# Kernel optimization log

Hardware: AMD Instinct MI355X
Metric: run time of the kernel (lower is better)

Reference implementation:

```python
import jax, jax.numpy as jnp
import numpy as np

IN_DIM = 64
OUT_DIM = 64
NUM_SPLINES = 8
DEGREE = 3
EPS = 1e-8


def setup_inputs() -> dict:
    key = jax.random.key(0)
    k1, k2 = jax.random.split(key, 2)
    x = jax.random.normal(k1, (4, 512, IN_DIM), dtype=jnp.float32)
    control_points = jax.random.normal(k2, (OUT_DIM, IN_DIM, NUM_SPLINES), dtype=jnp.float32) * 0.1
    K = NUM_SPLINES + DEGREE + 1  # 12 knots
    knots = jnp.broadcast_to(jnp.linspace(-1.0, 1.0, K, dtype=jnp.float32), (OUT_DIM, IN_DIM, K)).copy()
    activation_weights = jnp.ones((OUT_DIM, IN_DIM, 4), dtype=jnp.float32) / 4.0
    return {"x": x, "control_points": control_points, "knots": knots, "activation_weights": activation_weights}


def _bspline_basis(x, knots, degree):
    # x: (b, n, d); knots: (O, d, K) -> basis (b, O, n, d, K-degree-1)
    xs = x[:, None, :, :, None]          # (b, 1, n, d, 1)
    t = knots[None, :, None, :, :]       # (1, O, 1, d, K)
    # Cox-de Boor degree 0: indicator of half-open knot interval
    B = ((xs >= t[..., :-1]) & (xs < t[..., 1:])).astype(x.dtype)  # (b, O, n, d, K-1)
    for k in range(1, degree + 1):
        Km = B.shape[-1]
        c1 = (xs - t[..., : Km - 1]) / (t[..., k : k + Km - 1] - t[..., : Km - 1] + EPS)
        c2 = (t[..., k + 1 : k + Km] - xs) / (t[..., k + 1 : k + Km] - t[..., 1:Km] + EPS)
        B = c1 * B[..., :-1] + c2 * B[..., 1:]
    return B


def reference(x, control_points, knots, activation_weights):
    # B-spline branch: (b,O,n,d,S) x (O,d,S) -> (b,O,n)
    basis = _bspline_basis(x, knots, DEGREE)
    out = jnp.einsum('bonds,ods->bon', basis, control_points)
    # activation-mixture branch: activations are independent of the out dim
    acts = jnp.stack([jax.nn.relu(x), jnp.tanh(x), jax.nn.sigmoid(x), x], axis=-1)  # (b,n,d,4)
    act_out = jnp.einsum('bnda,oda->bon', acts, activation_weights)
    return out + 0.1 * act_out  # (b, out_dim, n)
```

## Files before the change

kernel.cpp:

```cpp
#include <hip/hip_runtime.h>

#define D_IN 64
#define D_OUT 64
#define NS 8
#define NK 12
#define NF 12
#define KTOT (D_IN * NF)
#define KAN_EPS 1e-8f
#define NBN 2048
#define KSPLIT 8
#define KCH (KTOT / KSPLIT)

__device__ int g_mism[16];

#define F_ELEMS  (KTOT * NBN)
#define WT_ELEMS (KTOT * D_OUT)

__device__ inline void basis8(float xv, const float* __restrict__ t, float* __restrict__ B)
{
    float Bb[11];
    #pragma unroll
    for (int i = 0; i < 11; ++i) Bb[i] = (xv >= t[i] && xv < t[i + 1]) ? 1.f : 0.f;
    #pragma unroll
    for (int i = 0; i < 10; ++i)
        Bb[i] = (xv - t[i]) * (1.f / (t[i + 1] - t[i] + KAN_EPS)) * Bb[i]
              + (t[i + 2] - xv) * (1.f / (t[i + 2] - t[i + 1] + KAN_EPS)) * Bb[i + 1];
    #pragma unroll
    for (int i = 0; i < 9; ++i)
        Bb[i] = (xv - t[i]) * (1.f / (t[i + 2] - t[i] + KAN_EPS)) * Bb[i]
              + (t[i + 3] - xv) * (1.f / (t[i + 3] - t[i + 1] + KAN_EPS)) * Bb[i + 1];
    #pragma unroll
    for (int i = 0; i < 8; ++i)
        Bb[i] = (xv - t[i]) * (1.f / (t[i + 3] - t[i] + KAN_EPS)) * Bb[i]
              + (t[i + 4] - xv) * (1.f / (t[i + 4] - t[i + 1] + KAN_EPS)) * Bb[i + 1];
    #pragma unroll
    for (int i = 0; i < 8; ++i) B[i] = Bb[i];
}

__global__ __launch_bounds__(256)
void kan_prep(const float* __restrict__ cp,
              const float* __restrict__ knots,
              const float* __restrict__ aw,
              const float* __restrict__ x,
              float* __restrict__ F,
              float* __restrict__ Wt)
{
    const int blk = blockIdx.x;
    const int tid = threadIdx.x;

    if (blk < 512) {
        const int idx = blk * 256 + tid;
        const int d  = idx >> 11;
        const int bn = idx & 2047;
        const float xv = x[bn * D_IN + d];

        float t[NK];
        #pragma unroll
        for (int j = 0; j < NK; ++j) t[j] = knots[d * NK + j];

        float B[8];
        basis8(xv, t, B);

        float* __restrict__ Fr = F + d * NF * NBN + bn;
        #pragma unroll
        for (int s = 0; s < 8; ++s) Fr[s * NBN] = B[s];

        const float v  = __expf(-xv);
        const float Ra = __builtin_amdgcn_rcpf(1.f + v * v);
        const float Rb = __builtin_amdgcn_rcpf(1.f + v);
        Fr[8  * NBN] = fmaxf(xv, 0.f);
        Fr[9  * NBN] = 2.f * Ra - 1.f;
        Fr[10 * NBN] = Rb;
        Fr[11 * NBN] = xv;

    } else {
        const int od = (blk - 512) * 256 + tid;
        const int o = od >> 6, d = od & 63;
        #pragma unroll
        for (int s = 0; s < 8; ++s) Wt[(d * NF + s) * D_OUT + o] = cp[od * NS + s];
        #pragma unroll
        for (int a = 0; a < 4; ++a) Wt[(d * NF + 8 + a) * D_OUT + o] = 0.1f * aw[od * 4 + a];

        int m = 0;
        #pragma unroll
        for (int j = 0; j < NK; ++j)
            m |= (knots[od * NK + j] != knots[d * NK + j]) ? 1 : 0;
        __shared__ int sm;
        if (tid == 0) sm = 0;
        __syncthreads();
        if (m) atomicOr(&sm, 1);
        __syncthreads();
        if (tid == 0) g_mism[blk - 512] = sm;
    }
}

__global__ __launch_bounds__(512)
void kan_gemm(const float* __restrict__ F,
              const float* __restrict__ Wt,
              const float* __restrict__ knots,
              const float* __restrict__ cp,
              const float* __restrict__ aw,
              const float* __restrict__ x,
              float* __restrict__ partial)
{
    const int lane = threadIdx.x & 63;
    const int og   = __builtin_amdgcn_readfirstlane(threadIdx.x >> 6);
    const int bn   = blockIdx.x * 64 + lane;
    const int ks   = blockIdx.y;

    float acc[8] = {0.f, 0.f, 0.f, 0.f, 0.f, 0.f, 0.f, 0.f};

    int mm = 0;
    #pragma unroll
    for (int k = 0; k < 16; ++k) mm |= g_mism[k];

    if (mm == 0) {
        const float* __restrict__ Fp = F  + (size_t)(ks * KCH) * NBN + bn;
        const float* __restrict__ Wp = Wt + (ks * KCH) * D_OUT + og * 8;
        #pragma unroll 8
        for (int k = 0; k < KCH; ++k) {
            const float f = Fp[(size_t)k * NBN];
            #pragma unroll
            for (int j = 0; j < 8; ++j)
                acc[j] = fmaf(f, Wp[k * D_OUT + j], acc[j]);
        }
    } else {
        for (int d = ks * (KCH / NF); d < ks * (KCH / NF) + (KCH / NF); ++d) {
            const float xv = x[bn * D_IN + d];
            const float v  = __expf(-xv);
            const float Ra = __builtin_amdgcn_rcpf(1.f + v * v);
            const float Rb = __builtin_amdgcn_rcpf(1.f + v);
            const float fr = fmaxf(xv, 0.f), fth = 2.f * Ra - 1.f;
            #pragma unroll
            for (int j = 0; j < 8; ++j) {
                const int o  = og * 8 + j;
                const int od = o * D_IN + d;
                float t[NK];
                #pragma unroll
                for (int jj = 0; jj < NK; ++jj) t[jj] = knots[od * NK + jj];
                float B[8];
                basis8(xv, t, B);
                float sp = 0.f;
                #pragma unroll
                for (int s = 0; s < NS; ++s) sp += B[s] * cp[od * NS + s];
                sp += 0.1f * (aw[od * 4 + 0] * fr + aw[od * 4 + 1] * fth
                            + aw[od * 4 + 2] * Rb + aw[od * 4 + 3] * xv);
                acc[j] += sp;
            }
        }
    }

    float* __restrict__ pp = partial + ((size_t)ks * D_OUT + og * 8) * NBN + bn;
    #pragma unroll
    for (int j = 0; j < 8; ++j) pp[(size_t)j * NBN] = acc[j];
}

__global__ __launch_bounds__(256)
void kan_reduce(const float4* __restrict__ partial, float* __restrict__ out)
{
    const int q = blockIdx.x * 256 + threadIdx.x;
    float4 s = partial[q];
    #pragma unroll
    for (int ks = 1; ks < KSPLIT; ++ks) {
        const float4 p = partial[(size_t)ks * (D_OUT * NBN / 4) + q];
        s.x += p.x; s.y += p.y; s.z += p.z; s.w += p.w;
    }
    const int idx = q * 4;
    const int o  = idx >> 11;
    const int bn = idx & 2047;
    const int b  = bn >> 9;
    const int n  = bn & 511;
    *(float4*)&out[(((b << 6) + o) << 9) + n] = s;
}

extern "C" void kernel_launch(void* const* d_in, const int* in_sizes, int n_in,
                              void* d_out, int out_size, void* d_ws, size_t ws_size,
                              hipStream_t stream) {
    const float* x     = (const float*)d_in[0];
    const float* cp    = (const float*)d_in[1];
    const float* knots = (const float*)d_in[2];
    const float* aw    = (const float*)d_in[3];
    float* out = (float*)d_out;

    float* F       = (float*)d_ws;
    float* Wt      = F + F_ELEMS;
    float* partial = Wt + WT_ELEMS;

    kan_prep<<<528, 256, 0, stream>>>(cp, knots, aw, x, F, Wt);

    dim3 ggrid(NBN / 64, KSPLIT);
    kan_gemm<<<ggrid, 512, 0, stream>>>(F, Wt, knots, cp, aw, x, partial);

    kan_reduce<<<128, 256, 0, stream>>>((const float4*)partial, out);
}
```

Baseline: 24.55 us.

## Fuse prep, GEMM and reduce into one kernel with shared-memory tiles

The three launches (feature/weight prep, split-K GEMM, reduction) become one kernel. Each block builds its basis features and transposed weight slice directly in shared memory, runs the split-K GEMM from LDS, and the last block per bn-tile (found with an atomic counter) reduces the partials and writes the output. This removes two kernel launches and the global round-trip of the F and Wt buffers. In exchange, the knot-mismatch check becomes per-block over only its own d slice, and each block redundantly recomputes its weight slice.

Result: slower. 25.46 us (+3.7%).

```diff
diff --git a/kernel.cpp b/kernel.cpp
--- a/kernel.cpp
+++ b/kernel.cpp
@@ -5,16 +5,17 @@
 #define NS 8
 #define NK 12
 #define NF 12
-#define KTOT (D_IN * NF)
-#define KAN_EPS 1e-8f
 #define NBN 2048
 #define KSPLIT 8
-#define KCH (KTOT / KSPLIT)
+#define DCH 8
+#define KCH (DCH * NF)
+#define BNT 64
+#define NT (NBN / BNT)
+#define KAN_EPS 1e-8f
 
-__device__ int g_mism[16];
+__device__ int g_cnt[NT];
 
-#define F_ELEMS  (KTOT * NBN)
-#define WT_ELEMS (KTOT * D_OUT)
+__device__ inline float rcp_(float a) { return __builtin_amdgcn_rcpf(a); }
 
 __device__ inline void basis8(float xv, const float* __restrict__ t, float* __restrict__ B)
 {
@@ -23,123 +24,114 @@
     for (int i = 0; i < 11; ++i) Bb[i] = (xv >= t[i] && xv < t[i + 1]) ? 1.f : 0.f;
     #pragma unroll
     for (int i = 0; i < 10; ++i)
-        Bb[i] = (xv - t[i]) * (1.f / (t[i + 1] - t[i] + KAN_EPS)) * Bb[i]
-              + (t[i + 2] - xv) * (1.f / (t[i + 2] - t[i + 1] + KAN_EPS)) * Bb[i + 1];
+        Bb[i] = (xv - t[i]) * rcp_(t[i + 1] - t[i] + KAN_EPS) * Bb[i]
+              + (t[i + 2] - xv) * rcp_(t[i + 2] - t[i + 1] + KAN_EPS) * Bb[i + 1];
     #pragma unroll
     for (int i = 0; i < 9; ++i)
-        Bb[i] = (xv - t[i]) * (1.f / (t[i + 2] - t[i] + KAN_EPS)) * Bb[i]
-              + (t[i + 3] - xv) * (1.f / (t[i + 3] - t[i + 1] + KAN_EPS)) * Bb[i + 1];
+        Bb[i] = (xv - t[i]) * rcp_(t[i + 2] - t[i] + KAN_EPS) * Bb[i]
+              + (t[i + 3] - xv) * rcp_(t[i + 3] - t[i + 1] + KAN_EPS) * Bb[i + 1];
     #pragma unroll
     for (int i = 0; i < 8; ++i)
-        Bb[i] = (xv - t[i]) * (1.f / (t[i + 3] - t[i] + KAN_EPS)) * Bb[i]
-              + (t[i + 4] - xv) * (1.f / (t[i + 4] - t[i + 1] + KAN_EPS)) * Bb[i + 1];
+        Bb[i] = (xv - t[i]) * rcp_(t[i + 3] - t[i] + KAN_EPS) * Bb[i]
+              + (t[i + 4] - xv) * rcp_(t[i + 4] - t[i + 1] + KAN_EPS) * Bb[i + 1];
     #pragma unroll
     for (int i = 0; i < 8; ++i) B[i] = Bb[i];
 }
 
-__global__ __launch_bounds__(256)
-void kan_prep(const float* __restrict__ cp,
-              const float* __restrict__ knots,
-              const float* __restrict__ aw,
-              const float* __restrict__ x,
-              float* __restrict__ F,
-              float* __restrict__ Wt)
+__global__ __launch_bounds__(512)
+void kan_fused(const float* __restrict__ x,
+               const float* __restrict__ cp,
+               const float* __restrict__ knots,
+               const float* __restrict__ aw,
+               float* __restrict__ partial,
+               float* __restrict__ out)
 {
-    const int blk = blockIdx.x;
-    const int tid = threadIdx.x;
+    __shared__ float sF[KCH][BNT];
+    __shared__ float sW[KCH][D_OUT];
+    __shared__ int s_mism, s_last;
 
-    if (blk < 512) {
-        const int idx = blk * 256 + tid;
-        const int d  = idx >> 11;
-        const int bn = idx & 2047;
+    const int bt   = blockIdx.x;
+    const int ks   = blockIdx.y;
+    const int tid  = threadIdx.x;
+    const int lane = tid & 63;
+    const int wv   = __builtin_amdgcn_readfirstlane(tid >> 6);
+    const int d0   = ks * DCH;
+    const int bn   = bt * BNT + lane;
+
+    if (tid == 0) { s_mism = 0; }
+    __syncthreads();
+
+    {
+        const int d = d0 + wv;
         const float xv = x[bn * D_IN + d];
-
         float t[NK];
         #pragma unroll
         for (int j = 0; j < NK; ++j) t[j] = knots[d * NK + j];
-
         float B[8];
         basis8(xv, t, B);
+        #pragma unroll
+        for (int s = 0; s < 8; ++s) sF[wv * NF + s][lane] = B[s];
+        const float v = __expf(-xv);
+        sF[wv * NF + 8][lane]  = fmaxf(xv, 0.f);
+        sF[wv * NF + 9][lane]  = 2.f * rcp_(1.f + v * v) - 1.f;
+        sF[wv * NF + 10][lane] = rcp_(1.f + v);
+        sF[wv * NF + 11][lane] = xv;
+    }
 
-        float* __restrict__ Fr = F + d * NF * NBN + bn;
-        #pragma unroll
-        for (int s = 0; s < 8; ++s) Fr[s * NBN] = B[s];
-
-        const float v  = __expf(-xv);
-        const float Ra = __builtin_amdgcn_rcpf(1.f + v * v);
-        const float Rb = __builtin_amdgcn_rcpf(1.f + v);
-        Fr[8  * NBN] = fmaxf(xv, 0.f);
-        Fr[9  * NBN] = 2.f * Ra - 1.f;
-        Fr[10 * NBN] = Rb;
-        Fr[11 * NBN] = xv;
-
-    } else {
-        const int od = (blk - 512) * 256 + tid;
-        const int o = od >> 6, d = od & 63;
-        #pragma unroll
-        for (int s = 0; s < 8; ++s) Wt[(d * NF + s) * D_OUT + o] = cp[od * NS + s];
-        #pragma unroll
-        for (int a = 0; a < 4; ++a) Wt[(d * NF + 8 + a) * D_OUT + o] = 0.1f * aw[od * 4 + a];
+    {
+        const int dg = tid >> 6;
+        const int o  = lane;
+        const int d  = d0 + dg;
+        const int od = o * D_IN + d;
+        const float4 c0 = *(const float4*)&cp[od * NS];
+        const float4 c1 = *(const float4*)&cp[od * NS + 4];
+        const float4 av = *(const float4*)&aw[od * 4];
+        sW[dg * NF + 0][o] = c0.x;  sW[dg * NF + 1][o] = c0.y;
+        sW[dg * NF + 2][o] = c0.z;  sW[dg * NF + 3][o] = c0.w;
+        sW[dg * NF + 4][o] = c1.x;  sW[dg * NF + 5][o] = c1.y;
+        sW[dg * NF + 6][o] = c1.z;  sW[dg * NF + 7][o] = c1.w;
+        sW[dg * NF + 8][o]  = 0.1f * av.x;
+        sW[dg * NF + 9][o]  = 0.1f * av.y;
+        sW[dg * NF + 10][o] = 0.1f * av.z;
+        sW[dg * NF + 11][o] = 0.1f * av.w;
 
         int m = 0;
         #pragma unroll
         for (int j = 0; j < NK; ++j)
             m |= (knots[od * NK + j] != knots[d * NK + j]) ? 1 : 0;
-        __shared__ int sm;
-        if (tid == 0) sm = 0;
-        __syncthreads();
-        if (m) atomicOr(&sm, 1);
-        __syncthreads();
-        if (tid == 0) g_mism[blk - 512] = sm;
+        if (m) atomicOr(&s_mism, 1);
     }
-}
+    __syncthreads();
 
-__global__ __launch_bounds__(512)
-void kan_gemm(const float* __restrict__ F,
-              const float* __restrict__ Wt,
-              const float* __restrict__ knots,
-              const float* __restrict__ cp,
-              const float* __restrict__ aw,
-              const float* __restrict__ x,
-              float* __restrict__ partial)
-{
-    const int lane = threadIdx.x & 63;
-    const int og   = __builtin_amdgcn_readfirstlane(threadIdx.x >> 6);
-    const int bn   = blockIdx.x * 64 + lane;
-    const int ks   = blockIdx.y;
-
+    const int og8 = __builtin_amdgcn_readfirstlane(wv * 8);
     float acc[8] = {0.f, 0.f, 0.f, 0.f, 0.f, 0.f, 0.f, 0.f};
 
-    int mm = 0;
-    #pragma unroll
-    for (int k = 0; k < 16; ++k) mm |= g_mism[k];
-
-    if (mm == 0) {
-        const float* __restrict__ Fp = F  + (size_t)(ks * KCH) * NBN + bn;
-        const float* __restrict__ Wp = Wt + (ks * KCH) * D_OUT + og * 8;
-        #pragma unroll 8
+    if (s_mism == 0) {
+        #pragma unroll 4
         for (int k = 0; k < KCH; ++k) {
-            const float f = Fp[(size_t)k * NBN];
-            #pragma unroll
-            for (int j = 0; j < 8; ++j)
-                acc[j] = fmaf(f, Wp[k * D_OUT + j], acc[j]);
+            const float f   = sF[k][lane];
+            const float4 wA = *(const float4*)&sW[k][og8];
+            const float4 wB = *(const float4*)&sW[k][og8 + 4];
+            acc[0] = fmaf(f, wA.x, acc[0]);  acc[1] = fmaf(f, wA.y, acc[1]);
+            acc[2] = fmaf(f, wA.z, acc[2]);  acc[3] = fmaf(f, wA.w, acc[3]);
+            acc[4] = fmaf(f, wB.x, acc[4]);  acc[5] = fmaf(f, wB.y, acc[5]);
+            acc[6] = fmaf(f, wB.z, acc[6]);  acc[7] = fmaf(f, wB.w, acc[7]);
         }
     } else {
-        for (int d = ks * (KCH / NF); d < ks * (KCH / NF) + (KCH / NF); ++d) {
+        for (int dg = 0; dg < DCH; ++dg) {
+            const int d = d0 + dg;
             const float xv = x[bn * D_IN + d];
             const float v  = __expf(-xv);
-            const float Ra = __builtin_amdgcn_rcpf(1.f + v * v);
-            const float Rb = __builtin_amdgcn_rcpf(1.f + v);
+            const float Ra = rcp_(1.f + v * v), Rb = rcp_(1.f + v);
             const float fr = fmaxf(xv, 0.f), fth = 2.f * Ra - 1.f;
-            #pragma unroll
             for (int j = 0; j < 8; ++j) {
-                const int o  = og * 8 + j;
+                const int o  = og8 + j;
                 const int od = o * D_IN + d;
-                float t[NK];
+                float t2[NK];
                 #pragma unroll
-                for (int jj = 0; jj < NK; ++jj) t[jj] = knots[od * NK + jj];
+                for (int jj = 0; jj < NK; ++jj) t2[jj] = knots[od * NK + jj];
                 float B[8];
-                basis8(xv, t, B);
+                basis8(xv, t2, B);
                 float sp = 0.f;
                 #pragma unroll
                 for (int s = 0; s < NS; ++s) sp += B[s] * cp[od * NS + s];
@@ -150,27 +142,30 @@
         }
     }
 
-    float* __restrict__ pp = partial + ((size_t)ks * D_OUT + og * 8) * NBN + bn;
     #pragma unroll
-    for (int j = 0; j < 8; ++j) pp[(size_t)j * NBN] = acc[j];
-}
+    for (int j = 0; j < 8; ++j)
+        partial[(size_t)(ks * D_OUT + og8 + j) * NBN + bn] = acc[j];
 
-__global__ __launch_bounds__(256)
-void kan_reduce(const float4* __restrict__ partial, float* __restrict__ out)
-{
-    const int q = blockIdx.x * 256 + threadIdx.x;
-    float4 s = partial[q];
+    __syncthreads();
+    if (tid == 0) {
+        __threadfence();
+        s_last = (atomicAdd(&g_cnt[bt], 1) == KSPLIT - 1);
+    }
+    __syncthreads();
+    if (!s_last) return;
+
+    if (tid == 0) g_cnt[bt] = 0;
+    __threadfence();
     #pragma unroll
-    for (int ks = 1; ks < KSPLIT; ++ks) {
-        const float4 p = partial[(size_t)ks * (D_OUT * NBN / 4) + q];
-        s.x += p.x; s.y += p.y; s.z += p.z; s.w += p.w;
+    for (int j = 0; j < 8; ++j) {
+        float s = 0.f;
+        #pragma unroll
+        for (int q = 0; q < KSPLIT; ++q)
+            s += partial[(size_t)(q * D_OUT + og8 + j) * NBN + bn];
+        const int b = bn >> 9;
+        const int n = bn & 511;
+        out[((b * D_OUT + og8 + j) << 9) | n] = s;
     }
-    const int idx = q * 4;
-    const int o  = idx >> 11;
-    const int bn = idx & 2047;
-    const int b  = bn >> 9;
-    const int n  = bn & 511;
-    *(float4*)&out[(((b << 6) + o) << 9) + n] = s;
 }
 
 extern "C" void kernel_launch(void* const* d_in, const int* in_sizes, int n_in,
@@ -180,16 +175,9 @@
     const float* cp    = (const float*)d_in[1];
     const float* knots = (const float*)d_in[2];
     const float* aw    = (const float*)d_in[3];
-    float* out = (float*)d_out;
+    float* out     = (float*)d_out;
+    float* partial = (float*)d_ws;
 
-    float* F       = (float*)d_ws;
-    float* Wt      = F + F_ELEMS;
-    float* partial = Wt + WT_ELEMS;
-
-    kan_prep<<<528, 256, 0, stream>>>(cp, knots, aw, x, F, Wt);
-
-    dim3 ggrid(NBN / 64, KSPLIT);
-    kan_gemm<<<ggrid, 512, 0, stream>>>(F, Wt, knots, cp, aw, x, partial);
-
-    kan_reduce<<<128, 256, 0, stream>>>((const float4*)partial, out);
+    dim3 grid(NT, KSPLIT);
+    kan_fused<<<grid, 512, 0, stream>>>(x, cp, knots, aw, partial, out);
 }
```
